# Kernel optimization log

Measured on AMD Instinct MI355X. Metric: run time of the kernel, lower is better.

The kernel has to match this reference:

```python
import jax, jax.numpy as jnp
import numpy as np


def setup_inputs() -> dict:
    key = jax.random.key(0)
    k1, k2 = jax.random.split(key)
    B, L, D = 16, 4096, 1024
    X = jax.random.normal(k1, (B, L, D), dtype=jnp.float32)
    G = jax.random.normal(k2, (D, 2), dtype=jnp.float32) * (1.0 / np.sqrt(D))
    Gb = jnp.zeros((2,), dtype=jnp.float32)
    return {"X": X, "G": G, "Gb": Gb}


def reference(X, G, Gb):
    # X: (B, L, D) with L = 2*maxseg. For even i in [0, L-3]:
    #   out_p = X[:,i] * g0 + X[:,i+2] * g1, gates g = softmax(X[:,i+1] @ G + Gb)
    L = X.shape[1]
    lefts = X[:, 0:L - 2:2, :]   # (B, P, D), P = L/2 - 1
    mids = X[:, 1:L - 1:2, :]    # (B, P, D)
    rights = X[:, 2:L:2, :]      # (B, P, D)
    gates = jax.nn.softmax(jnp.einsum('bpd,dg->bpg', mids, G) + Gb, axis=-1)  # (B, P, 2)
    out = lefts * gates[..., 0:1] + rights * gates[..., 1:2]  # (B, P, D)
    return out
```

## Files before the change

kernel.cpp:

```cpp
#include <hip/hip_runtime.h>
#include <hip/hip_bf16.h>

constexpr int B = 16;
constexpr int L = 4096;
constexpr int D = 1024;
constexpr int P = (L - 2) / 2;

__global__ __launch_bounds__(256) void gated_cnn_kernel(
    const float* __restrict__ X,
    const float* __restrict__ G,
    const float* __restrict__ Gb,
    float* __restrict__ out) {
  const int idx = blockIdx.x;
  const int b = idx / P;
  const int p = idx - b * P;

  const float* xb    = X + (size_t)b * L * D;
  const float* left  = xb + (size_t)(2 * p + 0) * D;
  const float* mid   = xb + (size_t)(2 * p + 1) * D;
  const float* right = xb + (size_t)(2 * p + 2) * D;
  float* o = out + (size_t)idx * D;

  const int t = threadIdx.x;

  const float4 m  = ((const float4*)mid)[t];
  const float4 lf = ((const float4*)left)[t];
  const float4 rt = ((const float4*)right)[t];
  const float4 gA = ((const float4*)G)[2 * t];
  const float4 gB = ((const float4*)G)[2 * t + 1];

  float s0 = m.x * gA.x + m.y * gA.z + m.z * gB.x + m.w * gB.z;
  float s1 = m.x * gA.y + m.y * gA.w + m.z * gB.y + m.w * gB.w;

  #pragma unroll
  for (int off = 32; off > 0; off >>= 1) {
    s0 += __shfl_down(s0, off, 64);
    s1 += __shfl_down(s1, off, 64);
  }

  __shared__ float red[8];
  const int wave = t >> 6;
  if ((t & 63) == 0) {
    red[wave * 2 + 0] = s0;
    red[wave * 2 + 1] = s1;
  }
  __syncthreads();

  float t0 = red[0] + red[2] + red[4] + red[6] + Gb[0];
  float t1 = red[1] + red[3] + red[5] + red[7] + Gb[1];
  const float mx = fmaxf(t0, t1);
  const float e0 = __expf(t0 - mx);
  const float e1 = __expf(t1 - mx);
  const float inv = 1.0f / (e0 + e1);
  const float g0 = e0 * inv;
  const float g1 = e1 * inv;

  float4 r;
  r.x = lf.x * g0 + rt.x * g1;
  r.y = lf.y * g0 + rt.y * g1;
  r.z = lf.z * g0 + rt.z * g1;
  r.w = lf.w * g0 + rt.w * g1;
  ((float4*)o)[t] = r;
}

extern "C" void kernel_launch(void* const* d_in, const int* in_sizes, int n_in,
                              void* d_out, int out_size, void* d_ws, size_t ws_size,
                              hipStream_t stream) {
  const float* X  = (const float*)d_in[0];
  const float* G  = (const float*)d_in[1];
  const float* Gb = (const float*)d_in[2];
  float* out = (float*)d_out;

  gated_cnn_kernel<<<dim3(B * P), dim3(256), 0, stream>>>(X, G, Gb, out);
}
```

Baseline: 383.4 us.

## Process chunks of rows per wave, reusing right row as next left

Restructures the kernel so each 64-lane wave handles four consecutive output rows of one batch instead of one 256-thread block per row. The right row of one step is carried in registers as the next step's left row. This removes the redundant global read of shared rows, the LDS reduction and __syncthreads, and the per-row reload of G. The reduction becomes a wave-only xor shuffle. The cost is fewer threads in flight (2048 blocks instead of ~32K) and serial dependent loads inside each wave, which could reduce memory-level parallelism.

```diff
diff --git a/kernel.cpp b/kernel.cpp
--- a/kernel.cpp
+++ b/kernel.cpp
@@ -6,61 +6,89 @@
 constexpr int D = 1024;
 constexpr int P = (L - 2) / 2;
 
+constexpr int WAVES_PER_BATCH = 512;
+constexpr int CHUNK = 4;
+
 __global__ __launch_bounds__(256) void gated_cnn_kernel(
     const float* __restrict__ X,
     const float* __restrict__ G,
     const float* __restrict__ Gb,
     float* __restrict__ out) {
-  const int idx = blockIdx.x;
-  const int b = idx / P;
-  const int p = idx - b * P;
+  const int gtid = blockIdx.x * 256 + threadIdx.x;
+  const int wid  = gtid >> 6;
+  const int lane = gtid & 63;
 
-  const float* xb    = X + (size_t)b * L * D;
-  const float* left  = xb + (size_t)(2 * p + 0) * D;
-  const float* mid   = xb + (size_t)(2 * p + 1) * D;
-  const float* right = xb + (size_t)(2 * p + 2) * D;
-  float* o = out + (size_t)idx * D;
+  const int b  = wid >> 9;
+  const int c  = wid & (WAVES_PER_BATCH - 1);
+  const int p0 = c * CHUNK;
 
-  const int t = threadIdx.x;
+  float4 gA[4], gB[4];
+  #pragma unroll
+  for (int j = 0; j < 4; ++j) {
+    const int f4 = j * 64 + lane;
+    gA[j] = ((const float4*)G)[2 * f4];
+    gB[j] = ((const float4*)G)[2 * f4 + 1];
+  }
+  const float gb0 = Gb[0];
+  const float gb1 = Gb[1];
 
-  const float4 m  = ((const float4*)mid)[t];
-  const float4 lf = ((const float4*)left)[t];
-  const float4 rt = ((const float4*)right)[t];
-  const float4 gA = ((const float4*)G)[2 * t];
-  const float4 gB = ((const float4*)G)[2 * t + 1];
+  const float* xb = X + (size_t)b * L * D;
+  float* ob = out + (size_t)b * P * D;
 
-  float s0 = m.x * gA.x + m.y * gA.z + m.z * gB.x + m.w * gB.z;
-  float s1 = m.x * gA.y + m.y * gA.w + m.z * gB.y + m.w * gB.w;
-
-  #pragma unroll
-  for (int off = 32; off > 0; off >>= 1) {
-    s0 += __shfl_down(s0, off, 64);
-    s1 += __shfl_down(s1, off, 64);
+  float4 lf[4];
+  {
+    const float4* lrow = (const float4*)(xb + (size_t)(2 * p0) * D);
+    #pragma unroll
+    for (int j = 0; j < 4; ++j) lf[j] = lrow[j * 64 + lane];
   }
 
-  __shared__ float red[8];
-  const int wave = t >> 6;
-  if ((t & 63) == 0) {
-    red[wave * 2 + 0] = s0;
-    red[wave * 2 + 1] = s1;
+  for (int i = 0; i < CHUNK; ++i) {
+    const int p = p0 + i;
+    if (p >= P) break;
+
+    const float4* mrow = (const float4*)(xb + (size_t)(2 * p + 1) * D);
+    const float4* rrow = (const float4*)(xb + (size_t)(2 * p + 2) * D);
+    float4 m[4], rt[4];
+    #pragma unroll
+    for (int j = 0; j < 4; ++j) {
+      m[j]  = mrow[j * 64 + lane];
+      rt[j] = rrow[j * 64 + lane];
+    }
+
+    float s0 = 0.f, s1 = 0.f;
+    #pragma unroll
+    for (int j = 0; j < 4; ++j) {
+      s0 += m[j].x * gA[j].x + m[j].y * gA[j].z + m[j].z * gB[j].x + m[j].w * gB[j].z;
+      s1 += m[j].x * gA[j].y + m[j].y * gA[j].w + m[j].z * gB[j].y + m[j].w * gB[j].w;
+    }
+
+    #pragma unroll
+    for (int off = 1; off < 64; off <<= 1) {
+      s0 += __shfl_xor(s0, off, 64);
+      s1 += __shfl_xor(s1, off, 64);
+    }
+
+    const float t0 = s0 + gb0;
+    const float t1 = s1 + gb1;
+    const float mx = fmaxf(t0, t1);
+    const float e0 = __expf(t0 - mx);
+    const float e1 = __expf(t1 - mx);
+    const float inv = 1.0f / (e0 + e1);
+    const float g0 = e0 * inv;
+    const float g1 = e1 * inv;
+
+    float4* orow = (float4*)(ob + (size_t)p * D);
+    #pragma unroll
+    for (int j = 0; j < 4; ++j) {
+      float4 r;
+      r.x = lf[j].x * g0 + rt[j].x * g1;
+      r.y = lf[j].y * g0 + rt[j].y * g1;
+      r.z = lf[j].z * g0 + rt[j].z * g1;
+      r.w = lf[j].w * g0 + rt[j].w * g1;
+      orow[j * 64 + lane] = r;
+      lf[j] = rt[j];
+    }
   }
-  __syncthreads();
-
-  float t0 = red[0] + red[2] + red[4] + red[6] + Gb[0];
-  float t1 = red[1] + red[3] + red[5] + red[7] + Gb[1];
-  const float mx = fmaxf(t0, t1);
-  const float e0 = __expf(t0 - mx);
-  const float e1 = __expf(t1 - mx);
-  const float inv = 1.0f / (e0 + e1);
-  const float g0 = e0 * inv;
-  const float g1 = e1 * inv;
-
-  float4 r;
-  r.x = lf.x * g0 + rt.x * g1;
-  r.y = lf.y * g0 + rt.y * g1;
-  r.z = lf.z * g0 + rt.z * g1;
-  r.w = lf.w * g0 + rt.w * g1;
-  ((float4*)o)[t] = r;
 }
 
 extern "C" void kernel_launch(void* const* d_in, const int* in_sizes, int n_in,
@@ -71,5 +99,5 @@
   const float* Gb = (const float*)d_in[2];
   float* out = (float*)d_out;
 
-  gated_cnn_kernel<<<dim3(B * P), dim3(256), 0, stream>>>(X, G, Gb, out);
+  gated_cnn_kernel<<<dim3(B * WAVES_PER_BATCH / 4), dim3(256), 0, stream>>>(X, G, Gb, out);
 }
```

Measured after the change: 388.5 us. About the same (+1.3%).
